# Kernel tuning notes

Hardware: AMD Instinct MI355X
Metric: run time of the kernel (lower is better)

The kernel has to match this reference:

```python
import jax, jax.numpy as jnp
import numpy as np


def apply_rope(x):
    # x: [B, T, H, D]
    T, D = x.shape[1], x.shape[3]
    inv_freq = 1.0 / (10000.0 ** (jnp.arange(0, D, 2, dtype=jnp.float32) / D))  # [D/2]
    t = jnp.arange(T, dtype=jnp.float32)
    freqs = jnp.outer(t, inv_freq)  # [T, D/2]
    sin_f = jnp.sin(freqs)[None, :, None, :]
    cos_f = jnp.cos(freqs)[None, :, None, :]
    x1, x2 = jnp.split(x, 2, axis=-1)
    return jnp.concatenate([x1 * cos_f - x2 * sin_f, x1 * sin_f + x2 * cos_f], axis=-1)


def setup_inputs() -> dict:
    key = jax.random.key(0)
    ks = jax.random.split(key, 5)
    B, T, D = 8, 8192, 128
    s = 1.0 / np.sqrt(D)
    return {
        "x": jax.random.normal(ks[0], (B, T, D), dtype=jnp.float32),
        "Wq": jax.random.normal(ks[1], (D, D), dtype=jnp.float32) * s,
        "bq": jnp.zeros((D,), dtype=jnp.float32),
        "Wk": jax.random.normal(ks[2], (D, D), dtype=jnp.float32) * s,
        "bk": jnp.zeros((D,), dtype=jnp.float32),
        "Wv": jax.random.normal(ks[3], (D, D), dtype=jnp.float32) * s,
        "bv": jnp.zeros((D,), dtype=jnp.float32),
        "Wo": jax.random.normal(ks[4], (D, D), dtype=jnp.float32) * s,
        "bo": jnp.zeros((D,), dtype=jnp.float32),
    }


def reference(x, Wq, bq, Wk, bk, Wv, bv, Wo, bo):
    n_heads = 8
    B, T, d_model = x.shape
    head_dim = d_model // n_heads

    q = (x @ Wq + bq).reshape(B, T, n_heads, head_dim)
    k = (x @ Wk + bk).reshape(B, T, n_heads, head_dim)
    v = (x @ Wv + bv).reshape(B, T, n_heads, head_dim)

    q = jax.nn.elu(apply_rope(q)) + 1.0
    k = jax.nn.elu(apply_rope(k)) + 1.0

    # non-causal linear attention: context = sum_t k_t v_t^T per head
    context = jnp.einsum("bthd,bthe->bhde", k, v)            # [B,H,Dh,Dh]
    out = jnp.einsum("bthd,bhde->bthe", q, context)           # [B,T,H,Dh]
    k_sum = jnp.sum(k, axis=1)                                  # [B,H,Dh]
    z = 1.0 / (jnp.einsum("bthd,bhd->bth", q, k_sum) + 1e-6)  # [B,T,H]
    out = out * z[..., None]

    out = out.reshape(B, T, d_model)
    return out @ Wo + bo
```

## Files before the change

### kernel.cpp

```cpp
#include <hip/hip_runtime.h>
#include <hip/hip_bf16.h>


typedef __attribute__((ext_vector_type(8))) short short8;
typedef __attribute__((ext_vector_type(4))) float floatx4;

#define DEV __device__ __forceinline__
#define MFMA __builtin_amdgcn_mfma_f32_16x16x32_bf16

DEV unsigned short bfh(float f) {
  unsigned int x = __float_as_uint(f);
  x += 0x7fffu + ((x >> 16) & 1u);
  return (unsigned short)(x >> 16);
}
DEV float bfdec(unsigned short u) { return __uint_as_float(((unsigned int)u) << 16); }
DEV void splitf(float f, unsigned short& h, unsigned short& l) {
  h = bfh(f);
  l = bfh(f - bfdec(h));
}

DEV void xpose_frag(floatx4 m0, floatx4 m1, int lane16, int quad,
                    short8& hi, short8& lo) {
  union { short8 s; unsigned short u[8]; } H, L;
#pragma unroll
  for (int j = 0; j < 8; ++j) {
    int srcLane = lane16 + (((quad & 1) * 2 + (j >> 2)) << 4);
    float vA = __shfl(m0[j & 3], srcLane, 64);
    float vB = __shfl(m1[j & 3], srcLane, 64);
    float v = (quad < 2) ? vA : vB;
    splitf(v, H.u[j], L.u[j]);
  }
  hi = H.s; lo = L.s;
}

DEV void async16(const void* g, void* l) {
  __builtin_amdgcn_global_load_lds(
      (const __attribute__((address_space(1))) unsigned int*)g,
      (__attribute__((address_space(3))) unsigned int*)l, 16, 0, 0);
}

__global__ void k_prep(const float* __restrict__ Wq, const float* __restrict__ Wk,
                       const float* __restrict__ Wv,
                       unsigned short* __restrict__ WTh, unsigned short* __restrict__ WTl,
                       float* __restrict__ ctxz, float2* __restrict__ ropeT) {
  int gid = blockIdx.x * 256 + threadIdx.x;
  if (gid < 6144) {
    int mat = gid >> 11, r = gid & 2047, n = r >> 4, k0 = (r & 15) * 8;
    const float* W = (mat == 0) ? Wq : (mat == 1) ? Wk : Wv;
    union { uint4 q; unsigned short u[8]; } oh, ol;
#pragma unroll
    for (int i = 0; i < 8; ++i) splitf(W[(size_t)(k0 + i) * 128 + n], oh.u[i], ol.u[i]);
    *(uint4*)&WTh[mat * 16384 + n * 128 + k0] = oh.q;
    *(uint4*)&WTl[mat * 16384 + n * 128 + k0] = ol.q;
  } else if (gid < 6144 + 17408) {
    ctxz[gid - 6144] = 0.0f;
  } else if (gid < 6144 + 17408 + 65536) {
    int r = gid - 23552;
    int t = r >> 3, j = r & 7;
    float invf = 1.0f / powf(10000.0f, (float)j * 0.125f);
    float s, c;
    sincosf((float)t * invf, &s, &c);
    ropeT[r] = make_float2(c, s);
  }
}

__global__ __launch_bounds__(512) void k_qkv(
    const float* __restrict__ x, const float2* __restrict__ ropeT,
    const unsigned short* __restrict__ WTh, const unsigned short* __restrict__ WTl,
    const float* __restrict__ bq, const float* __restrict__ bk, const float* __restrict__ bv,
    float* __restrict__ ctx, float* __restrict__ ksum,
    unsigned short* __restrict__ qws) {
  __shared__ unsigned short xh[64 * 136];
  __shared__ float rc[64][9], rs[64][9];
  const int tid = threadIdx.x;
  const int row0 = blockIdx.x * 64;
  const int b = row0 >> 13;
  const int t0 = row0 & 8191;

  {
    int r = tid >> 3, j = tid & 7;
    float2 cs = ropeT[(t0 + r) * 8 + j];
    rc[r][j] = cs.x; rs[r][j] = cs.y;
  }
  {
    int r = tid >> 3, cg = (tid & 7) * 16;
    const float* xp = x + (size_t)(row0 + r) * 128 + cg;
    float4 a = *(const float4*)xp;
    float4 b4 = *(const float4*)(xp + 4);
    float4 c4 = *(const float4*)(xp + 8);
    float4 d4 = *(const float4*)(xp + 12);
    float v[16] = {a.x, a.y, a.z, a.w, b4.x, b4.y, b4.z, b4.w,
                   c4.x, c4.y, c4.z, c4.w, d4.x, d4.y, d4.z, d4.w};
    union { short8 s; unsigned short u[8]; } h0, h1;
#pragma unroll
    for (int i = 0; i < 8; ++i) { h0.u[i] = bfh(v[i]); h1.u[i] = bfh(v[8 + i]); }
    *(short8*)&xh[r * 136 + cg] = h0.s;
    *(short8*)&xh[r * 136 + cg + 8] = h1.s;
  }
  __syncthreads();

  const int l = tid & 63, w = tid >> 6;
  const int lane16 = l & 15, quad = l >> 4;

  floatx4 acc[3][4];
#pragma unroll
  for (int i = 0; i < 3; ++i)
#pragma unroll
    for (int j = 0; j < 4; ++j) acc[i][j] = (floatx4){0.f, 0.f, 0.f, 0.f};

  size_t wbase[3];
#pragma unroll
  for (int mat = 0; mat < 3; ++mat)
    wbase[mat] = (size_t)mat * 16384 + (size_t)(w * 16 + lane16) * 128 + quad * 8;

  short8 wh[2][3], wl[2][3];
#pragma unroll
  for (int mat = 0; mat < 3; ++mat) {
    wh[0][mat] = *(const short8*)(WTh + wbase[mat]);
    wl[0][mat] = *(const short8*)(WTl + wbase[mat]);
  }

#pragma unroll
  for (int ks = 0; ks < 4; ++ks) {
    const int cur = ks & 1, nxt = cur ^ 1;
    if (ks < 3) {
#pragma unroll
      for (int mat = 0; mat < 3; ++mat) {
        wh[nxt][mat] = *(const short8*)(WTh + wbase[mat] + (ks + 1) * 32);
        wl[nxt][mat] = *(const short8*)(WTl + wbase[mat] + (ks + 1) * 32);
      }
    }
    short8 afh[4];
#pragma unroll
    for (int mt = 0; mt < 4; ++mt)
      afh[mt] = *(const short8*)&xh[(mt * 16 + lane16) * 136 + ks * 32 + quad * 8];
#pragma unroll
    for (int mat = 0; mat < 3; ++mat) {
#pragma unroll
      for (int mt = 0; mt < 4; ++mt) {
        acc[mat][mt] = MFMA(afh[mt], wh[cur][mat], acc[mat][mt], 0, 0, 0);
        acc[mat][mt] = MFMA(afh[mt], wl[cur][mat], acc[mat][mt], 0, 0, 0);
      }
    }
  }

  {
    int col = w * 16 + lane16;
    float bias[3] = {bq[col], bk[col], bv[col]};
#pragma unroll
    for (int mat = 0; mat < 3; ++mat)
#pragma unroll
      for (int mt = 0; mt < 4; ++mt)
#pragma unroll
        for (int r = 0; r < 4; ++r) acc[mat][mt][r] += bias[mat];
  }

  {
    const int d = lane16, j = d & 7;
#pragma unroll
    for (int mt = 0; mt < 4; ++mt) {
      float cc[4], ss[4];
#pragma unroll
      for (int r = 0; r < 4; ++r) {
        int tl = mt * 16 + quad * 4 + r;
        cc[r] = rc[tl][j]; ss[r] = rs[tl][j];
      }
#pragma unroll
      for (int mat = 0; mat < 2; ++mat) {
#pragma unroll
        for (int r = 0; r < 4; ++r) {
          float v = acc[mat][mt][r];
          float p = __shfl_xor(v, 8);
          float nv = (d < 8) ? (v * cc[r] - p * ss[r]) : (p * ss[r] + v * cc[r]);
          acc[mat][mt][r] = (nv > 0.f) ? (nv + 1.f) : __expf(nv);
        }
      }
    }
  }

  {
    float s = 0.f;
#pragma unroll
    for (int mt = 0; mt < 4; ++mt)
#pragma unroll
      for (int r = 0; r < 4; ++r) s += acc[1][mt][r];
    s += __shfl_xor(s, 16);
    s += __shfl_xor(s, 32);
    if (l < 16) atomicAdd(&ksum[(b * 8 + w) * 16 + lane16], s);
  }

#pragma unroll
  for (int mt = 0; mt < 4; ++mt)
#pragma unroll
    for (int r = 0; r < 4; ++r)
      qws[(size_t)(row0 + mt * 16 + quad * 4 + r) * 128 + w * 16 + lane16] =
          bfh(acc[0][mt][r]);

  {
    floatx4 c = (floatx4){0.f, 0.f, 0.f, 0.f};
#pragma unroll
    for (int ks2 = 0; ks2 < 2; ++ks2) {
      short8 kh, kl, vh, vl;
      xpose_frag(acc[1][ks2 * 2], acc[1][ks2 * 2 + 1], lane16, quad, kh, kl);
      xpose_frag(acc[2][ks2 * 2], acc[2][ks2 * 2 + 1], lane16, quad, vh, vl);
      c = MFMA(kh, vh, c, 0, 0, 0);
      c = MFMA(kl, vh, c, 0, 0, 0);
      c = MFMA(kh, vl, c, 0, 0, 0);
    }
#pragma unroll
    for (int r = 0; r < 4; ++r)
      atomicAdd(&ctx[((size_t)(b * 8 + w) * 16 + quad * 4 + r) * 16 + lane16], c[r]);
  }
}

__global__ void k_mprep(const float* __restrict__ Wo, const float* __restrict__ ctx,
                        unsigned short* __restrict__ MTh, unsigned short* __restrict__ MTl) {
  int gid = blockIdx.x * 256 + threadIdx.x;
  int b = gid >> 11, r = gid & 2047, oc = r >> 4, qcg = r & 15;
  int h = qcg >> 1, d0 = (qcg & 1) * 8;
  const float* C = ctx + (size_t)(b * 8 + h) * 256;
  float m[8] = {0.f, 0.f, 0.f, 0.f, 0.f, 0.f, 0.f, 0.f};
#pragma unroll 4
  for (int e = 0; e < 16; ++e) {
    float wv = Wo[(size_t)(h * 16 + e) * 128 + oc];
#pragma unroll
    for (int i = 0; i < 8; ++i) m[i] += C[(d0 + i) * 16 + e] * wv;
  }
  union { uint4 q; unsigned short u[8]; } oh, ol;
#pragma unroll
  for (int i = 0; i < 8; ++i) splitf(m[i], oh.u[i], ol.u[i]);
  int grp = (((oc >> 4) * 4 + (qcg >> 2)) * 64) + (qcg & 3) * 16 + (oc & 15);
  *(uint4*)&MTh[(size_t)b * 16384 + grp * 8] = oh.q;
  *(uint4*)&MTl[(size_t)b * 16384 + grp * 8] = ol.q;
}

__global__ __launch_bounds__(512) void k_zout(
    const unsigned short* __restrict__ qws,
    const unsigned short* __restrict__ MTh, const unsigned short* __restrict__ MTl,
    const float* __restrict__ bo, const float* __restrict__ ksum,
    float* __restrict__ out) {
  __shared__ __align__(16) unsigned short mh[16384], ml[16384];
  __shared__ float ksumS[128], boS[128];
  const int tid = threadIdx.x;
  const int row0 = blockIdx.x * 128;
  const int b = row0 >> 13;
  const int l = tid & 63, w = tid >> 6;
  const int lane16 = l & 15, quad = l >> 4;

  {
    const char* gh = (const char*)(MTh + (size_t)b * 16384);
    const char* gl = (const char*)(MTl + (size_t)b * 16384);
#pragma unroll
    for (int i = 0; i < 4; ++i) {
      int off = (i * 8 + w) * 1024 + l * 16;
      async16(gh + off, (char*)mh + off);
      async16(gl + off, (char*)ml + off);
    }
  }
  if (tid < 128) ksumS[tid] = ksum[b * 128 + tid];
  else if (tid < 256) boS[tid - 128] = bo[tid - 128];
  __syncthreads();

  const int trow = row0 + w * 16 + lane16;
  short8 ah[4], al[4];
#pragma unroll
  for (int ks = 0; ks < 4; ++ks) {
    union { short8 s8; unsigned short u[8]; } qq;
    qq.s8 = *(const short8*)&qws[(size_t)trow * 128 + ks * 32 + quad * 8];
    int kb = ks * 32 + quad * 8;
    float s = 0.f;
#pragma unroll
    for (int j = 0; j < 8; ++j) s += bfdec(qq.u[j]) * ksumS[kb + j];
    s += __shfl_xor(s, 16);
    float z = 1.0f / (s + 1e-6f);
    union { short8 s8; unsigned short u[8]; } H, L;
#pragma unroll
    for (int j = 0; j < 8; ++j) splitf(bfdec(qq.u[j]) * z, H.u[j], L.u[j]);
    ah[ks] = H.s8;
    al[ks] = L.s8;
  }

  floatx4 oacc[8];
#pragma unroll
  for (int j = 0; j < 8; ++j) oacc[j] = (floatx4){0.f, 0.f, 0.f, 0.f};

#pragma unroll
  for (int nt = 0; nt < 8; ++nt) {
#pragma unroll
    for (int ks = 0; ks < 4; ++ks) {
      int moff = ((nt * 4 + ks) * 64 + l) * 8;
      short8 wbh = *(const short8*)&mh[moff];
      short8 wbl = *(const short8*)&ml[moff];
      oacc[nt] = MFMA(ah[ks], wbh, oacc[nt], 0, 0, 0);
      oacc[nt] = MFMA(al[ks], wbh, oacc[nt], 0, 0, 0);
      oacc[nt] = MFMA(ah[ks], wbl, oacc[nt], 0, 0, 0);
    }
  }

#pragma unroll
  for (int nt = 0; nt < 8; ++nt) {
    int oc = nt * 16 + lane16;
    float bb = boS[oc];
#pragma unroll
    for (int r = 0; r < 4; ++r) {
      int t = row0 + w * 16 + quad * 4 + r;
      out[(size_t)t * 128 + oc] = oacc[nt][r] + bb;
    }
  }
}

extern "C" void kernel_launch(void* const* d_in, const int* in_sizes, int n_in,
                              void* d_out, int out_size, void* d_ws, size_t ws_size,
                              hipStream_t stream) {
  const float* x  = (const float*)d_in[0];
  const float* Wq = (const float*)d_in[1];
  const float* bq = (const float*)d_in[2];
  const float* Wk = (const float*)d_in[3];
  const float* bk = (const float*)d_in[4];
  const float* Wv = (const float*)d_in[5];
  const float* bv = (const float*)d_in[6];
  const float* Wo = (const float*)d_in[7];
  const float* bo = (const float*)d_in[8];
  float* out = (float*)d_out;

  unsigned short* qws = (unsigned short*)d_ws;
  unsigned short* WTh = qws + 8388608;
  unsigned short* WTl = WTh + 49152;
  float* ctx  = (float*)(WTl + 49152);
  float* ksum = ctx + 16384;
  unsigned short* MTh = (unsigned short*)(ksum + 1024);
  unsigned short* MTl = MTh + 131072;
  float2* ropeT = (float2*)(MTl + 131072);

  k_prep<<<348, 256, 0, stream>>>(Wq, Wk, Wv, WTh, WTl, ctx, ropeT);
  k_qkv<<<1024, 512, 0, stream>>>(x, ropeT, WTh, WTl, bq, bk, bv, ctx, ksum, qws);
  k_mprep<<<64, 256, 0, stream>>>(Wo, ctx, MTh, MTl);
  k_zout<<<512, 512, 0, stream>>>(qws, MTh, MTl, bo, ksum, out);
}
```

Baseline: 159.8 us.

## Fuse Wo-context premultiply into output kernel and stage stores through LDS

Removes the separate k_mprep launch. Each k_zout block now recomputes the per-batch context·Wo matrix from ctx held in shared memory and splits it into bf16 hi/lo directly in LDS. Both k_qkv (bf16 q) and k_zout (fp32 output) now stage results through shared memory so global stores are coalesced 16-byte rows. The cost is redundant recomputation of the 128x128 product in each of the 512 blocks, plus extra barriers.

```diff
diff --git a/kernel.cpp b/kernel.cpp
--- a/kernel.cpp
+++ b/kernel.cpp
@@ -31,12 +31,6 @@
     splitf(v, H.u[j], L.u[j]);
   }
   hi = H.s; lo = L.s;
-}
-
-DEV void async16(const void* g, void* l) {
-  __builtin_amdgcn_global_load_lds(
-      (const __attribute__((address_space(1))) unsigned int*)g,
-      (__attribute__((address_space(3))) unsigned int*)l, 16, 0, 0);
 }
 
 __global__ void k_prep(const float* __restrict__ Wq, const float* __restrict__ Wk,
@@ -177,6 +171,14 @@
       }
     }
   }
+  __syncthreads();
+
+  unsigned short* qS = xh;
+#pragma unroll
+  for (int mt = 0; mt < 4; ++mt)
+#pragma unroll
+    for (int r = 0; r < 4; ++r)
+      qS[(mt * 16 + quad * 4 + r) * 136 + w * 16 + lane16] = bfh(acc[0][mt][r]);
 
   {
     float s = 0.f;
@@ -188,13 +190,6 @@
     s += __shfl_xor(s, 32);
     if (l < 16) atomicAdd(&ksum[(b * 8 + w) * 16 + lane16], s);
   }
-
-#pragma unroll
-  for (int mt = 0; mt < 4; ++mt)
-#pragma unroll
-    for (int r = 0; r < 4; ++r)
-      qws[(size_t)(row0 + mt * 16 + quad * 4 + r) * 128 + w * 16 + lane16] =
-          bfh(acc[0][mt][r]);
 
   {
     floatx4 c = (floatx4){0.f, 0.f, 0.f, 0.f};
@@ -211,35 +206,24 @@
     for (int r = 0; r < 4; ++r)
       atomicAdd(&ctx[((size_t)(b * 8 + w) * 16 + quad * 4 + r) * 16 + lane16], c[r]);
   }
-}
-
-__global__ void k_mprep(const float* __restrict__ Wo, const float* __restrict__ ctx,
-                        unsigned short* __restrict__ MTh, unsigned short* __restrict__ MTl) {
-  int gid = blockIdx.x * 256 + threadIdx.x;
-  int b = gid >> 11, r = gid & 2047, oc = r >> 4, qcg = r & 15;
-  int h = qcg >> 1, d0 = (qcg & 1) * 8;
-  const float* C = ctx + (size_t)(b * 8 + h) * 256;
-  float m[8] = {0.f, 0.f, 0.f, 0.f, 0.f, 0.f, 0.f, 0.f};
-#pragma unroll 4
-  for (int e = 0; e < 16; ++e) {
-    float wv = Wo[(size_t)(h * 16 + e) * 128 + oc];
-#pragma unroll
-    for (int i = 0; i < 8; ++i) m[i] += C[(d0 + i) * 16 + e] * wv;
-  }
-  union { uint4 q; unsigned short u[8]; } oh, ol;
-#pragma unroll
-  for (int i = 0; i < 8; ++i) splitf(m[i], oh.u[i], ol.u[i]);
-  int grp = (((oc >> 4) * 4 + (qcg >> 2)) * 64) + (qcg & 3) * 16 + (oc & 15);
-  *(uint4*)&MTh[(size_t)b * 16384 + grp * 8] = oh.q;
-  *(uint4*)&MTl[(size_t)b * 16384 + grp * 8] = ol.q;
+  __syncthreads();
+
+  {
+    int r = tid >> 3, c = (tid & 7) * 16;
+    uint4 a0 = *(const uint4*)&qS[r * 136 + c];
+    uint4 a1 = *(const uint4*)&qS[r * 136 + c + 8];
+    *(uint4*)&qws[(size_t)(row0 + r) * 128 + c] = a0;
+    *(uint4*)&qws[(size_t)(row0 + r) * 128 + c + 8] = a1;
+  }
 }
 
 __global__ __launch_bounds__(512) void k_zout(
     const unsigned short* __restrict__ qws,
-    const unsigned short* __restrict__ MTh, const unsigned short* __restrict__ MTl,
-    const float* __restrict__ bo, const float* __restrict__ ksum,
+    const float* __restrict__ Wo, const float* __restrict__ bo,
+    const float* __restrict__ ctx, const float* __restrict__ ksum,
     float* __restrict__ out) {
   __shared__ __align__(16) unsigned short mh[16384], ml[16384];
+  __shared__ float ctxS[2048];
   __shared__ float ksumS[128], boS[128];
   const int tid = threadIdx.x;
   const int row0 = blockIdx.x * 128;
@@ -248,17 +232,44 @@
   const int lane16 = l & 15, quad = l >> 4;
 
   {
-    const char* gh = (const char*)(MTh + (size_t)b * 16384);
-    const char* gl = (const char*)(MTl + (size_t)b * 16384);
-#pragma unroll
-    for (int i = 0; i < 4; ++i) {
-      int off = (i * 8 + w) * 1024 + l * 16;
-      async16(gh + off, (char*)mh + off);
-      async16(gl + off, (char*)ml + off);
-    }
+    float4 c4 = *(const float4*)(ctx + (size_t)b * 2048 + tid * 4);
+    *(float4*)&ctxS[tid * 4] = c4;
   }
   if (tid < 128) ksumS[tid] = ksum[b * 128 + tid];
   else if (tid < 256) boS[tid - 128] = bo[tid - 128];
+  __syncthreads();
+
+  {
+    int oc = tid & 127;
+    int qcg0 = (tid >> 7) * 4;
+#pragma unroll
+    for (int hh = 0; hh < 2; ++hh) {
+      int h = (qcg0 >> 1) + hh;
+      float m0[8] = {0, 0, 0, 0, 0, 0, 0, 0};
+      float m1[8] = {0, 0, 0, 0, 0, 0, 0, 0};
+#pragma unroll 4
+      for (int e = 0; e < 16; ++e) {
+        float wv = Wo[(size_t)(h * 16 + e) * 128 + oc];
+        const float* cp = ctxS + h * 256 + e;
+#pragma unroll
+        for (int i = 0; i < 8; ++i) {
+          m0[i] += cp[i * 16] * wv;
+          m1[i] += cp[(8 + i) * 16] * wv;
+        }
+      }
+#pragma unroll
+      for (int half = 0; half < 2; ++half) {
+        int qcg = qcg0 + hh * 2 + half;
+        const float* mm = half ? m1 : m0;
+        union { uint4 q; unsigned short u[8]; } oh, ol;
+#pragma unroll
+        for (int i = 0; i < 8; ++i) splitf(mm[i], oh.u[i], ol.u[i]);
+        int grp = (((oc >> 4) * 4 + (qcg >> 2)) * 64) + (qcg & 3) * 16 + (oc & 15);
+        *(uint4*)&mh[grp * 8] = oh.q;
+        *(uint4*)&ml[grp * 8] = ol.q;
+      }
+    }
+  }
   __syncthreads();
 
   const int trow = row0 + w * 16 + lane16;
@@ -296,15 +307,24 @@
       oacc[nt] = MFMA(ah[ks], wbl, oacc[nt], 0, 0, 0);
     }
   }
-
+  __syncthreads();
+
+  float* outW = (float*)((char*)mh + w * 8192);
 #pragma unroll
   for (int nt = 0; nt < 8; ++nt) {
-    int oc = nt * 16 + lane16;
-    float bb = boS[oc];
-#pragma unroll
-    for (int r = 0; r < 4; ++r) {
-      int t = row0 + w * 16 + quad * 4 + r;
-      out[(size_t)t * 128 + oc] = oacc[nt][r] + bb;
+    float bb = boS[nt * 16 + lane16];
+#pragma unroll
+    for (int r = 0; r < 4; ++r)
+      outW[(quad * 4 + r) * 128 + nt * 16 + lane16] = oacc[nt][r] + bb;
+  }
+  __syncthreads();
+
+  {
+    int rr = l >> 2, c0 = (l & 3) * 4;
+#pragma unroll
+    for (int j = 0; j < 8; ++j) {
+      float4 v4 = *(const float4*)&outW[rr * 128 + c0 + j * 16];
+      *(float4*)&out[(size_t)(row0 + w * 16 + rr) * 128 + c0 + j * 16] = v4;
     }
   }
 }
@@ -328,12 +348,9 @@
   unsigned short* WTl = WTh + 49152;
   float* ctx  = (float*)(WTl + 49152);
   float* ksum = ctx + 16384;
-  unsigned short* MTh = (unsigned short*)(ksum + 1024);
-  unsigned short* MTl = MTh + 131072;
-  float2* ropeT = (float2*)(MTl + 131072);
+  float2* ropeT = (float2*)(ksum + 1024);
 
   k_prep<<<348, 256, 0, stream>>>(Wq, Wk, Wv, WTh, WTl, ctx, ropeT);
   k_qkv<<<1024, 512, 0, stream>>>(x, ropeT, WTh, WTl, bq, bk, bv, ctx, ksum, qws);
-  k_mprep<<<64, 256, 0, stream>>>(Wo, ctx, MTh, MTl);
-  k_zout<<<512, 512, 0, stream>>>(qws, MTh, MTl, bo, ksum, out);
-}
+  k_zout<<<512, 512, 0, stream>>>(qws, Wo, bo, ctx, ksum, out);
+}
```

After: 164.0 us. 1.03x slower.
